# Performance work log

Measured on AMD Instinct MI355X. Metric: run time of the kernel, lower is better.

The kernel has to match this reference:

```python
import jax, jax.numpy as jnp
import numpy as np

N_NODES = 50000
N_EDGES = 600000
D = 128

def _linear_params(key, fan_in, fan_out):
    # torch nn.Linear default init: U(-1/sqrt(fan_in), 1/sqrt(fan_in))
    k1, k2 = jax.random.split(key)
    bound = 1.0 / np.sqrt(fan_in)
    W = jax.random.uniform(k1, (fan_in, fan_out), minval=-bound, maxval=bound, dtype=jnp.float32)
    b = jax.random.uniform(k2, (fan_out,), minval=-bound, maxval=bound, dtype=jnp.float32)
    return W, b

def setup_inputs() -> dict:
    key = jax.random.key(0)
    kh, ke, k1, k2, k3, k4 = jax.random.split(key, 6)
    h = jax.random.normal(kh, (N_NODES, D), dtype=jnp.float32)
    edges = jax.random.randint(ke, (N_EDGES, 2), 0, N_NODES, dtype=jnp.int32)
    msg_W1, msg_b1 = _linear_params(k1, 2 * D, D)
    msg_W2, msg_b2 = _linear_params(k2, D, D)
    upd_W1, upd_b1 = _linear_params(k3, 2 * D, D)
    upd_W2, upd_b2 = _linear_params(k4, D, D)
    return {"h": h, "edges": edges,
            "msg_W1": msg_W1, "msg_b1": msg_b1, "msg_W2": msg_W2, "msg_b2": msg_b2,
            "upd_W1": upd_W1, "upd_b1": upd_b1, "upd_W2": upd_W2, "upd_b2": upd_b2}

def reference(h, edges, msg_W1, msg_b1, msg_W2, msg_b2, upd_W1, upd_b1, upd_W2, upd_b2):
    src = edges[:, 0]
    dst = edges[:, 1]
    # message MLP over concatenated [h_src, h_dst] per edge: [E, 2D] -> [E, D]
    pair = jnp.concatenate([h[src], h[dst]], axis=-1)
    msg = jax.nn.relu(pair @ msg_W1 + msg_b1) @ msg_W2 + msg_b2
    # scatter-add aggregate messages onto destination nodes: [N, D]
    agg = jax.ops.segment_sum(msg, dst, num_segments=h.shape[0])
    # update MLP on [h, agg]: [N, 2D] -> [N, D]
    upd_in = jnp.concatenate([h, agg], axis=-1)
    h_new = jax.nn.relu(upd_in @ upd_W1 + upd_b1) @ upd_W2 + upd_b2
    return h + h_new
```

## Files before the change

kernel.cpp:

```cpp
#include <hip/hip_runtime.h>
#include <hip/hip_bf16.h>

#define NN 50000
#define NE 600000
#define TN 64
#define NT ((NN + TN - 1) / TN)
#define CAP 1024

typedef unsigned short u16;
typedef unsigned int u32;
typedef unsigned long long u64;
typedef __attribute__((ext_vector_type(8))) short bf16x8;
typedef __attribute__((ext_vector_type(16))) float f32x16;
typedef __attribute__((ext_vector_type(4))) int int4v;

#define SM_AB   0
#define SM_MSGT 16384
#define SM_TT   32768
#define SM_SB   49152
#define SM_BIAS 65536
#define SMEM_TOTAL 66560

__device__ __forceinline__ void bar_lds() {
    asm volatile("s_waitcnt lgkmcnt(0)" ::: "memory");
    __builtin_amdgcn_s_barrier();
}

__device__ __forceinline__ u16 f2b(float x) {
    __hip_bfloat16 b = __float2bfloat16(x);
    union { __hip_bfloat16 b; u16 u; } c; c.b = b; return c.u;
}
__device__ __forceinline__ int4v zero4() {
    int4v v; v[0]=0; v[1]=0; v[2]=0; v[3]=0; return v;
}
__device__ __forceinline__ f32x16 zero16() {
    f32x16 z;
#pragma unroll
    for (int i = 0; i < 16; ++i) z[i] = 0.f;
    return z;
}
__device__ __forceinline__ int4v cvt8(const float* __restrict__ p) {
    const float4* q = (const float4*)p;
    float4 f0 = q[0], f1 = q[1];
    union { u16 u[8]; int4v v; } r;
    r.u[0]=f2b(f0.x); r.u[1]=f2b(f0.y); r.u[2]=f2b(f0.z); r.u[3]=f2b(f0.w);
    r.u[4]=f2b(f1.x); r.u[5]=f2b(f1.y); r.u[6]=f2b(f1.z); r.u[7]=f2b(f1.w);
    return r.v;
}
__device__ __forceinline__ u64 pack4(float a, float b, float c, float d) {
    union { u16 u[4]; u64 q; } r;
    r.u[0]=f2b(a); r.u[1]=f2b(b); r.u[2]=f2b(c); r.u[3]=f2b(d); return r.q;
}
__device__ __forceinline__ f32x16 mfma16(bf16x8 a, bf16x8 b, f32x16 c) {
    return __builtin_amdgcn_mfma_f32_32x32x16_bf16(a, b, c, 0, 0, 0);
}
__device__ __forceinline__ bf16x8 ld256(const char* base, int row, int c) {
    return *(const bf16x8*)(base + row * 256 + ((c ^ (row & 15)) << 4));
}
__device__ __forceinline__ bf16x8 ld128r(const char* base, int row, int c) {
    return *(const bf16x8*)(base + row * 128 + ((c ^ (row & 7)) << 4));
}

__global__ void prep_kernel(const float* __restrict__ h,
                            const float* __restrict__ W1m, const float* __restrict__ W2m,
                            const float* __restrict__ W1u, const float* __restrict__ W2u,
                            u16* __restrict__ w1tm, u16* __restrict__ w2tm,
                            u16* __restrict__ w1tu, u16* __restrict__ w2tu,
                            u16* __restrict__ hbuf, int do_h)
{
    int tid = blockIdx.x * blockDim.x + threadIdx.x;
    int stride = gridDim.x * blockDim.x;
    for (int i = tid; i < 128 * 256; i += stride) {
        int n = i >> 8, k = i & 255;
        w1tm[i] = f2b(W1m[k * 128 + n]);
        w1tu[i] = f2b(W1u[k * 128 + n]);
    }
    for (int i = tid; i < 128 * 128; i += stride) {
        int n = i >> 7, k = i & 127;
        w2tm[i] = f2b(W2m[k * 128 + n]);
        w2tu[i] = f2b(W2u[k * 128 + n]);
    }
    if (do_h) {
        for (int i = tid; i < NN * 128 / 8; i += stride)
            *(int4v*)(hbuf + (size_t)i * 8) = cvt8(h + (size_t)i * 8);
    }
}

__global__ __launch_bounds__(256) void scatter_kernel(
    const int* __restrict__ edges, u32* __restrict__ elist, int* __restrict__ cursor)
{
    __shared__ int lcnt[NT];
    const int e0 = blockIdx.x * 2048;
    for (int i = threadIdx.x; i < NT; i += 256) lcnt[i] = 0;
    __syncthreads();
#pragma unroll
    for (int k = 0; k < 8; ++k) {
        int e = e0 + k * 256 + threadIdx.x;
        if (e < NE) atomicAdd(&lcnt[edges[2 * e + 1] >> 6], 1);
    }
    __syncthreads();
    for (int i = threadIdx.x; i < NT; i += 256) {
        int cn = lcnt[i];
        if (cn > 0) lcnt[i] = atomicAdd(&cursor[i], cn);
    }
    __syncthreads();
#pragma unroll
    for (int k = 0; k < 8; ++k) {
        int e = e0 + k * 256 + threadIdx.x;
        if (e < NE) {
            int s = edges[2 * e], d = edges[2 * e + 1];
            int bin = d >> 6;
            int pos = atomicAdd(&lcnt[bin], 1);
            if (pos < CAP) elist[(size_t)bin * CAP + pos] = (u32)s | ((u32)(d & 63) << 16);
        }
    }
}

__global__ __launch_bounds__(256, 2) void fused_kernel(
    const float* __restrict__ h, const u16* __restrict__ hb, int use_hb,
    const u32* __restrict__ elist, const int* __restrict__ cursor,
    const u16* __restrict__ w1m, const u16* __restrict__ w2m,
    const u16* __restrict__ w1u, const u16* __restrict__ w2u,
    const float* __restrict__ b1m, const float* __restrict__ b2m,
    const float* __restrict__ b1u, const float* __restrict__ b2u,
    float* __restrict__ outp)
{
    extern __shared__ char sm[];
    char* ab   = sm + SM_AB;
    char* msgt = sm + SM_MSGT;
    char* tt   = sm + SM_TT;
    char* Sb   = sm + SM_SB;
    char* Stb  = sm + SM_SB + 8192;
    char* bias = sm + SM_BIAS;

    const int tid  = threadIdx.x;
    const int lane = tid & 63;
    const int wid  = tid >> 6;
    const int l31  = lane & 31;
    const int kg   = lane >> 5;
    const int nrow  = wid * 32 + l31;
    const int ecol0 = l31;
    const int ecol1 = 32 + l31;

    const int bin = blockIdx.x;
    const int n0  = bin * TN;
    int size = cursor[bin]; if (size > CAP) size = CAP;
    const u32* el = elist + (size_t)bin * CAP;
    const int nchunk = (size + 63) >> 6;

    bf16x8 w1f[8], w2f[8];
#pragma unroll
    for (int kk = 0; kk < 8; ++kk) {
        w1f[kk] = *(const bf16x8*)(w1m + nrow * 256 + (kk * 2 + kg) * 8);
        w2f[kk] = *(const bf16x8*)(w2m + nrow * 128 + (kk * 2 + kg) * 8);
    }
    const float b2ms = b2m[nrow];

    for (int i = tid; i < 1024; i += 256) {
        int row = i >> 4, c = i & 15;
        int node = n0 + row;
        int4v v = zero4();
        if (node < NN) {
            if (use_hb) v = *(const int4v*)(hb + (size_t)node * 128 + c * 8);
            else        v = cvt8(h + (size_t)node * 128 + c * 8);
        }
        *(int4v*)(msgt + row * 256 + ((c ^ (row & 15)) << 4)) = v;
    }
    if (tid < 32)      *(float4*)(bias + tid * 16)          = ((const float4*)b1m)[tid];
    else if (tid < 64) *(float4*)(bias + 512 + (tid-32)*16) = ((const float4*)b1u)[tid - 32];
    {
        char* z = sm + SM_SB + tid * 64;
        *(int4v*)z = zero4(); *(int4v*)(z + 16) = zero4();
        *(int4v*)(z + 32) = zero4(); *(int4v*)(z + 48) = zero4();
    }

    auto put_ones = [&](u32 rec, int cb2, u16 val) {
        if (cb2 + lane < size) {
            int d = (int)((rec >> 16) & 63);
            *(u16*)(Sb  + d * 128 + (((lane >> 3) ^ (d & 7)) << 4) + (lane & 7) * 2) = val;
            *(u16*)(Stb + lane * 128 + (((d >> 3) ^ (lane & 7)) << 4) + (d & 7) * 2) = val;
        }
    };

    const int s_row0 = tid >> 4, s_cc = tid & 15;
    auto stage_load = [&](u32 dle_c, int cb2, int4v* v) {
#pragma unroll
        for (int u = 0; u < 4; ++u) {
            int row = s_row0 + 16 * u;
            int s = ((int)__shfl((int)dle_c, row, 64)) & 0xFFFF;
            v[u] = zero4();
            if (cb2 + row < size)
                v[u] = use_hb ? *(const int4v*)(hb + (size_t)s * 128 + s_cc * 8)
                              : cvt8(h + (size_t)s * 128 + s_cc * 8);
        }
    };
    auto stage_write = [&](const int4v* v) {
#pragma unroll
        for (int u = 0; u < 4; ++u) {
            int row = s_row0 + 16 * u;
            *(int4v*)(ab + row * 256 + ((s_cc ^ (row & 15)) << 4)) = v[u];
        }
    };

    u32 dle = (lane < size) ? el[lane] : 0u;
    if (nchunk > 0) {
        int4v v[4];
        stage_load(dle, 0, v);
        stage_write(v);
    }
    __syncthreads();

    {
        f32x16 t0 = zero16(), t1 = zero16();
        __builtin_amdgcn_s_setprio(1);
#pragma unroll
        for (int kk = 0; kk < 8; ++kk) {
            bf16x8 wtf = *(const bf16x8*)(w1m + nrow * 256 + (16 + kk * 2 + kg) * 8);
            int ch = kk * 2 + kg;
            t0 = mfma16(wtf, ld256(msgt, ecol0, ch), t0);
            t1 = mfma16(wtf, ld256(msgt, ecol1, ch), t1);
        }
        __builtin_amdgcn_s_setprio(0);
#pragma unroll
        for (int r = 0; r < 16; ++r) {
            int n1 = wid * 32 + (r & 3) + 8 * (r >> 2) + 4 * kg;
            *(u16*)(tt + n1 * 128 + (((ecol0 >> 3) ^ (n1 & 7)) << 4) + (ecol0 & 7) * 2) = f2b(t0[r]);
            *(u16*)(tt + n1 * 128 + (((ecol1 >> 3) ^ (n1 & 7)) << 4) + (ecol1 & 7) * 2) = f2b(t1[r]);
        }
    }
    if (wid == 0) put_ones(dle, 0, 0x3F80);
    bar_lds();

    f32x16 aggT0 = zero16(), aggT1 = zero16();
    for (int c = 0; c < nchunk; ++c) {
        const int cb = c << 6;
        const bool havepf = (c + 1 < nchunk);

        u32 dle_next = (havepf && (cb + 64 + lane < size)) ? el[cb + 64 + lane] : 0u;

        f32x16 mm0 = zero16(), mm1 = zero16();
        __builtin_amdgcn_s_setprio(1);
#pragma unroll
        for (int kk = 0; kk < 4; ++kk) {
            int ch = kk * 2 + kg;
            bf16x8 ttf = ld128r(tt, nrow, ch);
            mm0 = mfma16(ttf, ld128r(Stb, ecol0, ch), mm0);
            mm1 = mfma16(ttf, ld128r(Stb, ecol1, ch), mm1);
        }
#pragma unroll
        for (int kk = 0; kk < 8; ++kk) {
            int ch = kk * 2 + kg;
            mm0 = mfma16(w1f[kk], ld256(ab, ecol0, ch), mm0);
            mm1 = mfma16(w1f[kk], ld256(ab, ecol1, ch), mm1);
        }
        __builtin_amdgcn_s_setprio(0);
        bar_lds();

#pragma unroll
        for (int rq = 0; rq < 4; ++rq) {
            float4 bq = *(const float4*)(bias + (wid * 32 + 8 * rq + 4 * kg) * 4);
            int cch = wid * 4 + rq;
            u64 q0 = pack4(fmaxf(mm0[4 * rq + 0] + bq.x, 0.f),
                           fmaxf(mm0[4 * rq + 1] + bq.y, 0.f),
                           fmaxf(mm0[4 * rq + 2] + bq.z, 0.f),
                           fmaxf(mm0[4 * rq + 3] + bq.w, 0.f));
            u64 q1 = pack4(fmaxf(mm1[4 * rq + 0] + bq.x, 0.f),
                           fmaxf(mm1[4 * rq + 1] + bq.y, 0.f),
                           fmaxf(mm1[4 * rq + 2] + bq.z, 0.f),
                           fmaxf(mm1[4 * rq + 3] + bq.w, 0.f));
            *(u64*)(ab + ecol0 * 256 + ((cch ^ (ecol0 & 15)) << 4) + 8 * kg) = q0;
            *(u64*)(ab + ecol1 * 256 + ((cch ^ (ecol1 & 15)) << 4) + 8 * kg) = q1;
        }
        bar_lds();

        int4v v[4];
        if (havepf) stage_load(dle_next, cb + 64, v);
        {
            f32x16 c20 = zero16(), c21 = zero16();
            __builtin_amdgcn_s_setprio(1);
#pragma unroll
            for (int kk = 0; kk < 8; ++kk) {
                int ch = kk * 2 + kg;
                c20 = mfma16(ld256(ab, ecol0, ch), w2f[kk], c20);
                c21 = mfma16(ld256(ab, ecol1, ch), w2f[kk], c21);
            }
            __builtin_amdgcn_s_setprio(0);
#pragma unroll
            for (int rq = 0; rq < 4; ++rq) {
                u64 q0 = pack4(c20[4 * rq + 0] + b2ms, c20[4 * rq + 1] + b2ms,
                               c20[4 * rq + 2] + b2ms, c20[4 * rq + 3] + b2ms);
                u64 q1 = pack4(c21[4 * rq + 0] + b2ms, c21[4 * rq + 1] + b2ms,
                               c21[4 * rq + 2] + b2ms, c21[4 * rq + 3] + b2ms);
                *(u64*)(msgt + nrow * 128 + ((rq ^ (nrow & 7)) << 4) + 8 * kg) = q0;
                *(u64*)(msgt + nrow * 128 + (((4 + rq) ^ (nrow & 7)) << 4) + 8 * kg) = q1;
            }
        }
        bar_lds();

        __builtin_amdgcn_s_setprio(1);
#pragma unroll
        for (int kk = 0; kk < 4; ++kk) {
            int ch = kk * 2 + kg;
            bf16x8 msf = ld128r(msgt, nrow, ch);
            aggT0 = mfma16(msf, ld128r(Sb, ecol0, ch), aggT0);
            aggT1 = mfma16(msf, ld128r(Sb, ecol1, ch), aggT1);
        }
        __builtin_amdgcn_s_setprio(0);
        if (havepf) stage_write(v);
        bar_lds();

        if (havepf) {
            if (wid == 0) {
                put_ones(dle, cb, 0);
                asm volatile("s_waitcnt lgkmcnt(0)" ::: "memory");
                put_ones(dle_next, cb + 64, 0x3F80);
            }
            bar_lds();
        }
        dle = dle_next;
    }

#pragma unroll
    for (int rq = 0; rq < 4; ++rq) {
        int cch = wid * 4 + rq;
        u64 q0 = pack4(aggT0[4 * rq + 0], aggT0[4 * rq + 1], aggT0[4 * rq + 2], aggT0[4 * rq + 3]);
        u64 q1 = pack4(aggT1[4 * rq + 0], aggT1[4 * rq + 1], aggT1[4 * rq + 2], aggT1[4 * rq + 3]);
        *(u64*)(ab + ecol0 * 256 + ((cch ^ (ecol0 & 15)) << 4) + 8 * kg) = q0;
        *(u64*)(ab + ecol1 * 256 + ((cch ^ (ecol1 & 15)) << 4) + 8 * kg) = q1;
    }
    for (int i = tid; i < 1024; i += 256) {
        int row = i >> 4, c = i & 15;
        int node = n0 + row;
        int4v v = zero4();
        if (node < NN) {
            if (use_hb) v = *(const int4v*)(hb + (size_t)node * 128 + c * 8);
            else        v = cvt8(h + (size_t)node * 128 + c * 8);
        }
        *(int4v*)(Sb + row * 256 + ((c ^ (row & 15)) << 4)) = v;
    }
    bar_lds();

    {
        f32x16 au0 = zero16(), au1 = zero16();
        {
            bf16x8 wa[8];
#pragma unroll
            for (int kk = 0; kk < 8; ++kk)
                wa[kk] = *(const bf16x8*)(w1u + nrow * 256 + (kk * 2 + kg) * 8);
            __builtin_amdgcn_s_setprio(1);
#pragma unroll
            for (int kk = 0; kk < 8; ++kk) {
                int ch = kk * 2 + kg;
                au0 = mfma16(wa[kk], ld256(Sb, ecol0, ch), au0);
                au1 = mfma16(wa[kk], ld256(Sb, ecol1, ch), au1);
            }
            __builtin_amdgcn_s_setprio(0);
        }
        {
            bf16x8 wbf[8];
#pragma unroll
            for (int kk = 0; kk < 8; ++kk)
                wbf[kk] = *(const bf16x8*)(w1u + nrow * 256 + ((8 + kk) * 2 + kg) * 8);
            __builtin_amdgcn_s_setprio(1);
#pragma unroll
            for (int kk = 0; kk < 8; ++kk) {
                int ch = kk * 2 + kg;
                au0 = mfma16(wbf[kk], ld256(ab, ecol0, ch), au0);
                au1 = mfma16(wbf[kk], ld256(ab, ecol1, ch), au1);
            }
            __builtin_amdgcn_s_setprio(0);
        }
#pragma unroll
        for (int rq = 0; rq < 4; ++rq) {
            float4 bq = *(const float4*)(bias + 512 + (wid * 32 + 8 * rq + 4 * kg) * 4);
            int cch = wid * 4 + rq;
            u64 q0 = pack4(fmaxf(au0[4 * rq + 0] + bq.x, 0.f),
                           fmaxf(au0[4 * rq + 1] + bq.y, 0.f),
                           fmaxf(au0[4 * rq + 2] + bq.z, 0.f),
                           fmaxf(au0[4 * rq + 3] + bq.w, 0.f));
            u64 q1 = pack4(fmaxf(au1[4 * rq + 0] + bq.x, 0.f),
                           fmaxf(au1[4 * rq + 1] + bq.y, 0.f),
                           fmaxf(au1[4 * rq + 2] + bq.z, 0.f),
                           fmaxf(au1[4 * rq + 3] + bq.w, 0.f));
            *(u64*)(msgt + ecol0 * 256 + ((cch ^ (ecol0 & 15)) << 4) + 8 * kg) = q0;
            *(u64*)(msgt + ecol1 * 256 + ((cch ^ (ecol1 & 15)) << 4) + 8 * kg) = q1;
        }
    }
    bar_lds();

    {
        bf16x8 wc[8];
#pragma unroll
        for (int kk = 0; kk < 8; ++kk)
            wc[kk] = *(const bf16x8*)(w2u + nrow * 128 + (kk * 2 + kg) * 8);
        const float b2us = b2u[nrow];
        f32x16 cu0 = zero16(), cu1 = zero16();
        __builtin_amdgcn_s_setprio(1);
#pragma unroll
        for (int kk = 0; kk < 8; ++kk) {
            int ch = kk * 2 + kg;
            cu0 = mfma16(ld256(msgt, ecol0, ch), wc[kk], cu0);
            cu1 = mfma16(ld256(msgt, ecol1, ch), wc[kk], cu1);
        }
        __builtin_amdgcn_s_setprio(0);
#pragma unroll
        for (int r = 0; r < 16; ++r) {
            int rmap = (r & 3) + 8 * (r >> 2) + 4 * kg;
            int ng0 = n0 + rmap;
            int ng1 = n0 + 32 + rmap;
            if (ng0 < NN) {
                size_t o = (size_t)ng0 * 128 + nrow;
                outp[o] = cu0[r] + b2us + h[o];
            }
            if (ng1 < NN) {
                size_t o = (size_t)ng1 * 128 + nrow;
                outp[o] = cu1[r] + b2us + h[o];
            }
        }
    }
}

extern "C" void kernel_launch(void* const* d_in, const int* in_sizes, int n_in,
                              void* d_out, int out_size, void* d_ws, size_t ws_size,
                              hipStream_t stream) {
    const float* h   = (const float*)d_in[0];
    const int* edges = (const int*)d_in[1];
    const float* W1m = (const float*)d_in[2];
    const float* b1m = (const float*)d_in[3];
    const float* W2m = (const float*)d_in[4];
    const float* b2m = (const float*)d_in[5];
    const float* W1u = (const float*)d_in[6];
    const float* b1u = (const float*)d_in[7];
    const float* W2u = (const float*)d_in[8];
    const float* b2u = (const float*)d_in[9];
    float* out = (float*)d_out;

    char* ws = (char*)d_ws;
    u16* w1tm  = (u16*)(ws + 0);
    u16* w2tm  = (u16*)(ws + 65536);
    u16* w1tu  = (u16*)(ws + 98304);
    u16* w2tu  = (u16*)(ws + 163840);
    int* curs  = (int*)(ws + 196608);
    u32* elist = (u32*)(ws + 200704);
    u16* hb    = (u16*)(ws + 3403776);
    int use_hb = (ws_size >= 3403776ull + (size_t)NN * 128 * 2) ? 1 : 0;

    (void)hipFuncSetAttribute((const void*)fused_kernel,
                              hipFuncAttributeMaxDynamicSharedMemorySize, SMEM_TOTAL);

    hipMemsetAsync(curs, 0, NT * sizeof(int), stream);
    prep_kernel<<<512, 256, 0, stream>>>(h, W1m, W2m, W1u, W2u,
                                         w1tm, w2tm, w1tu, w2tu, hb, use_hb);
    scatter_kernel<<<(NE + 2047) / 2048, 256, 0, stream>>>(edges, elist, curs);
    fused_kernel<<<NT, 256, SMEM_TOTAL, stream>>>(h, hb, use_hb, elist, curs,
                                                  w1tm, w2tm, w1tu, w2tu,
                                                  b1m, b2m, b1u, b2u, out);
}
```

Baseline: 166.4 us.

## Double-buffer scatter matrix to drop per-chunk barrier and hoist gather loads

The destination one-hot scatter matrix S is split into two ping-pong buffers (S0/S1) kept apart from its transpose. The next chunk's buffer is zeroed and filled during earlier phases, and the transpose is updated before the second-layer GEMM. This removes the fifth barrier and the serial put_ones phase at the end of each chunk iteration. The staging gather of the next chunk's source rows is also issued earlier, right after the first GEMM, to hide more of its latency. In exchange, LDS use grows by 8 KB per block, which may threaten the two-blocks-per-CU occupancy target.

```diff
diff --git a/kernel.cpp b/kernel.cpp
--- a/kernel.cpp
+++ b/kernel.cpp
@@ -17,9 +17,11 @@
 #define SM_AB   0
 #define SM_MSGT 16384
 #define SM_TT   32768
-#define SM_SB   49152
-#define SM_BIAS 65536
-#define SMEM_TOTAL 66560
+#define SM_ST   49152
+#define SM_S0   57344
+#define SM_S1   65536
+#define SM_BIAS 73728
+#define SMEM_TOTAL 74752
 
 __device__ __forceinline__ void bar_lds() {
     asm volatile("s_waitcnt lgkmcnt(0)" ::: "memory");
@@ -129,9 +131,11 @@
     char* ab   = sm + SM_AB;
     char* msgt = sm + SM_MSGT;
     char* tt   = sm + SM_TT;
-    char* Sb   = sm + SM_SB;
-    char* Stb  = sm + SM_SB + 8192;
+    char* Stb  = sm + SM_ST;
+    char* S0   = sm + SM_S0;
+    char* S1   = sm + SM_S1;
     char* bias = sm + SM_BIAS;
+    char* htu  = sm + SM_ST;
 
     const int tid  = threadIdx.x;
     const int lane = tid & 63;
@@ -169,16 +173,21 @@
     if (tid < 32)      *(float4*)(bias + tid * 16)          = ((const float4*)b1m)[tid];
     else if (tid < 64) *(float4*)(bias + 512 + (tid-32)*16) = ((const float4*)b1u)[tid - 32];
     {
-        char* z = sm + SM_SB + tid * 64;
+        char* z = sm + SM_ST + tid * 64;
         *(int4v*)z = zero4(); *(int4v*)(z + 16) = zero4();
         *(int4v*)(z + 32) = zero4(); *(int4v*)(z + 48) = zero4();
     }
 
-    auto put_ones = [&](u32 rec, int cb2, u16 val) {
+    auto put_St = [&](u32 rec, int cb2, u16 val) {
         if (cb2 + lane < size) {
             int d = (int)((rec >> 16) & 63);
-            *(u16*)(Sb  + d * 128 + (((lane >> 3) ^ (d & 7)) << 4) + (lane & 7) * 2) = val;
             *(u16*)(Stb + lane * 128 + (((d >> 3) ^ (lane & 7)) << 4) + (d & 7) * 2) = val;
+        }
+    };
+    auto put_S = [&](char* Sbuf, u32 rec, int cb2) {
+        if (cb2 + lane < size) {
+            int d = (int)((rec >> 16) & 63);
+            *(u16*)(Sbuf + d * 128 + (((lane >> 3) ^ (d & 7)) << 4) + (lane & 7) * 2) = 0x3F80;
         }
     };
 
@@ -228,13 +237,15 @@
             *(u16*)(tt + n1 * 128 + (((ecol1 >> 3) ^ (n1 & 7)) << 4) + (ecol1 & 7) * 2) = f2b(t1[r]);
         }
     }
-    if (wid == 0) put_ones(dle, 0, 0x3F80);
+    if (wid == 0) { put_St(dle, 0, 0x3F80); put_S(S0, dle, 0); }
     bar_lds();
 
     f32x16 aggT0 = zero16(), aggT1 = zero16();
     for (int c = 0; c < nchunk; ++c) {
         const int cb = c << 6;
         const bool havepf = (c + 1 < nchunk);
+        char* Scur = (c & 1) ? S1 : S0;
+        char* Snxt = (c & 1) ? S0 : S1;
 
         u32 dle_next = (havepf && (cb + 64 + lane < size)) ? el[cb + 64 + lane] : 0u;
 
@@ -256,6 +267,8 @@
         __builtin_amdgcn_s_setprio(0);
         bar_lds();
 
+        int4v v[4];
+        if (havepf) stage_load(dle_next, cb + 64, v);
 #pragma unroll
         for (int rq = 0; rq < 4; ++rq) {
             float4 bq = *(const float4*)(bias + (wid * 32 + 8 * rq + 4 * kg) * 4);
@@ -271,10 +284,17 @@
             *(u64*)(ab + ecol0 * 256 + ((cch ^ (ecol0 & 15)) << 4) + 8 * kg) = q0;
             *(u64*)(ab + ecol1 * 256 + ((cch ^ (ecol1 & 15)) << 4) + 8 * kg) = q1;
         }
+        if (havepf) {
+            char* z = Snxt + tid * 32;
+            *(int4v*)z = zero4(); *(int4v*)(z + 16) = zero4();
+            if (wid == 0) {
+                put_St(dle, cb, 0);
+                asm volatile("s_waitcnt lgkmcnt(0)" ::: "memory");
+                put_St(dle_next, cb + 64, 0x3F80);
+            }
+        }
         bar_lds();
 
-        int4v v[4];
-        if (havepf) stage_load(dle_next, cb + 64, v);
         {
             f32x16 c20 = zero16(), c21 = zero16();
             __builtin_amdgcn_s_setprio(1);
@@ -295,6 +315,7 @@
                 *(u64*)(msgt + nrow * 128 + (((4 + rq) ^ (nrow & 7)) << 4) + 8 * kg) = q1;
             }
         }
+        if (wid == 0 && havepf) put_S(Snxt, dle_next, cb + 64);
         bar_lds();
 
         __builtin_amdgcn_s_setprio(1);
@@ -302,21 +323,12 @@
         for (int kk = 0; kk < 4; ++kk) {
             int ch = kk * 2 + kg;
             bf16x8 msf = ld128r(msgt, nrow, ch);
-            aggT0 = mfma16(msf, ld128r(Sb, ecol0, ch), aggT0);
-            aggT1 = mfma16(msf, ld128r(Sb, ecol1, ch), aggT1);
+            aggT0 = mfma16(msf, ld128r(Scur, ecol0, ch), aggT0);
+            aggT1 = mfma16(msf, ld128r(Scur, ecol1, ch), aggT1);
         }
         __builtin_amdgcn_s_setprio(0);
         if (havepf) stage_write(v);
         bar_lds();
-
-        if (havepf) {
-            if (wid == 0) {
-                put_ones(dle, cb, 0);
-                asm volatile("s_waitcnt lgkmcnt(0)" ::: "memory");
-                put_ones(dle_next, cb + 64, 0x3F80);
-            }
-            bar_lds();
-        }
         dle = dle_next;
     }
 
@@ -336,7 +348,7 @@
             if (use_hb) v = *(const int4v*)(hb + (size_t)node * 128 + c * 8);
             else        v = cvt8(h + (size_t)node * 128 + c * 8);
         }
-        *(int4v*)(Sb + row * 256 + ((c ^ (row & 15)) << 4)) = v;
+        *(int4v*)(htu + row * 256 + ((c ^ (row & 15)) << 4)) = v;
     }
     bar_lds();
 
@@ -351,8 +363,8 @@
 #pragma unroll
             for (int kk = 0; kk < 8; ++kk) {
                 int ch = kk * 2 + kg;
-                au0 = mfma16(wa[kk], ld256(Sb, ecol0, ch), au0);
-                au1 = mfma16(wa[kk], ld256(Sb, ecol1, ch), au1);
+                au0 = mfma16(wa[kk], ld256(htu, ecol0, ch), au0);
+                au1 = mfma16(wa[kk], ld256(htu, ecol1, ch), au1);
             }
             __builtin_amdgcn_s_setprio(0);
         }
```

Result: no change. 165.9 us (-0.3%).
